# Performance work log

Hardware: AMD Instinct MI355X
Metric: run time of the kernel (lower is better)

Reference implementation:

```python
import jax, jax.numpy as jnp
import numpy as np

B = 1 << 20          # batch of independent integrator states
NC = 64              # RBF centers
DT = jnp.float32(0.005)
M_ = jnp.float32(1.0 / 95.45)
OFFST = jnp.float32(-3.2902)
F_V = jnp.float32(214.9261)
F_C = jnp.float32(19.3607)
A_COEF = (0.0, 0.5, 0.5, 1.0)  # RK stage offsets (module applies all to yddoti)


def setup_inputs() -> dict:
    key = jax.random.key(0)
    k1, k2, k3, k4, k5 = jax.random.split(key, 5)
    return {
        "inputs": jax.random.normal(k1, (B,), dtype=jnp.float32),     # control u per state
        "states": jax.random.normal(k2, (2, B), dtype=jnp.float32),   # ydot = states.view(2,-1)
        "centers": jax.random.normal(k3, (NC,), dtype=jnp.float32),
        "gammas": jax.random.uniform(k4, (NC,), dtype=jnp.float32),   # positive widths
        "weights": jax.random.normal(k5, (NC,), dtype=jnp.float32),
    }


def _rbf(x, centers, gammas, weights):
    # x: [B] -> Gaussian RBF features [B, NC] -> scalar output [B]
    d = x[:, None] - centers[None, :]
    phi = jnp.exp(-gammas[None, :] * d * d)
    return phi @ weights


def _fun(u, ydot, centers, gammas, weights):
    # (u_*u - F_v_@ydot - F_f_@ydot - C_*(offst + rbf(ydot[1]))) * M
    # row 0: -ydot[1];  row 1: u - F_v*ydot[1] - F_c*ydot[1] - (offst + rbf(ydot[1]))
    y1 = ydot[1]
    r = _rbf(y1, centers, gammas, weights)
    f0 = -y1
    f1 = u - F_V * y1 - F_C * y1 - (OFFST + r)
    return jnp.stack([f0, f1], axis=0) * M_


def reference(inputs, states, centers, gammas, weights):
    ydot = states.reshape(2, -1)  # [2, B]
    yddoti = _fun(inputs, ydot, centers, gammas, weights)
    # NOTE: faithful to source — every stage offsets from yddoti, not k_i
    ydoti = ydot + A_COEF[0] * yddoti * DT
    k1 = _fun(inputs, ydoti, centers, gammas, weights)
    ydot2 = ydot + A_COEF[1] * yddoti * DT
    k2 = _fun(inputs, ydot2, centers, gammas, weights)
    ydot3 = ydot + A_COEF[2] * yddoti * DT
    k3 = _fun(inputs, ydot3, centers, gammas, weights)
    ydot4 = ydot + A_COEF[3] * yddoti * DT
    k4 = _fun(inputs, ydot4, centers, gammas, weights)
    st_n = DT / 6.0 * (k1 + 2.0 * k2 + 2.0 * k3 + k4)
    return st_n  # [2, B]
```

## Files before the change

kernel.cpp:

```cpp
#include <hip/hip_runtime.h>


#define NTAB   256
#define XMIN   (-8.0f)
#define HSTEP  0.0625f
#define INVH   16.0f
#define TOFF   128.0f
#define SMAX   254.999f

__device__ __constant__ const float kM     = (float)(1.0 / 95.45);
__device__ __constant__ const float kOFFST = -3.2902f;
__device__ __constant__ const float kKK    = 214.9261f + 19.3607f;
__device__ __constant__ const float kC1    = (0.005f / 6.0f) * (float)(1.0 / 95.45);

__device__ __forceinline__ void rk_core(const float2* __restrict__ ltab,
                                        float u, float y1,
                                        float& o0, float& o1) {
    float s  = fmaf(y1, INVH, TOFF);
    s = fminf(fmaxf(s, 0.0f), SMAX);
    float fl = floorf(s);
    float fr = s - fl;
    float2 p = ltab[(int)fl];
    float r0 = fmaf(fr, p.y, p.x);
    float d1 = (fmaf(-kKK, y1, u) - (kOFFST + r0)) * kM;
    float t3 = (3.0f * 0.005f) * d1;
    float lin = fmaf(6.0f, y1, t3);
    o0 = -kC1 * lin;
    float rsum = fmaf(p.y * INVH, t3, 6.0f * r0);
    float acc  = fmaf(-kKK, lin, fmaf(6.0f, u, -6.0f * kOFFST)) - rsum;
    o1 = kC1 * acc;
}

template <int NC>
__global__ __launch_bounds__(256)
void rk_fused_kernel(const float* __restrict__ u_in,
                     const float* __restrict__ y1_in,
                     const float* __restrict__ centers,
                     const float* __restrict__ gammas,
                     const float* __restrict__ weights,
                     float* __restrict__ out, int B, int nc) {
    __shared__ float  vraw[NTAB];
    __shared__ float2 ltab[NTAB];
    const int tid = threadIdx.x;
    const long base = ((long)blockIdx.x * blockDim.x + tid) * 8;
    const bool full = (base + 8 <= (long)B);

    float4 ua, ub, ya, yb;
    if (full) {
        ua = *(const float4*)(u_in  + base);
        ub = *(const float4*)(u_in  + base + 4);
        ya = *(const float4*)(y1_in + base);
        yb = *(const float4*)(y1_in + base + 4);
    }

    {
        float x = XMIN + (float)tid * HSTEP;
        float v = 0.0f;
        if (NC > 0) {
            #pragma unroll
            for (int j = 0; j < NC; ++j) {
                float d = x - centers[j];
                v = fmaf(weights[j], __expf(-gammas[j] * d * d), v);
            }
        } else {
            for (int j = 0; j < nc; ++j) {
                float d = x - centers[j];
                v = fmaf(weights[j], __expf(-gammas[j] * d * d), v);
            }
        }
        vraw[tid] = v;
    }
    __syncthreads();
    {
        float v0 = vraw[tid];
        float sl = (tid < NTAB - 1) ? (vraw[tid + 1] - v0) : 0.0f;
        ltab[tid] = make_float2(v0, sl);
    }
    __syncthreads();

    if (full) {
        float uu[8] = {ua.x, ua.y, ua.z, ua.w, ub.x, ub.y, ub.z, ub.w};
        float yy[8] = {ya.x, ya.y, ya.z, ya.w, yb.x, yb.y, yb.z, yb.w};
        float o0[8], o1[8];
        #pragma unroll
        for (int e = 0; e < 8; ++e) rk_core(ltab, uu[e], yy[e], o0[e], o1[e]);
        *(float4*)(out + base)         = make_float4(o0[0], o0[1], o0[2], o0[3]);
        *(float4*)(out + base + 4)     = make_float4(o0[4], o0[5], o0[6], o0[7]);
        *(float4*)(out + B + base)     = make_float4(o1[0], o1[1], o1[2], o1[3]);
        *(float4*)(out + B + base + 4) = make_float4(o1[4], o1[5], o1[6], o1[7]);
    } else {
        for (long e = base; e < (long)B && e < base + 8; ++e) {
            float o0, o1;
            rk_core(ltab, u_in[e], y1_in[e], o0, o1);
            out[e] = o0;
            out[B + e] = o1;
        }
    }
}

extern "C" void kernel_launch(void* const* d_in, const int* in_sizes, int n_in,
                              void* d_out, int out_size, void* d_ws, size_t ws_size,
                              hipStream_t stream) {
    const float* u       = (const float*)d_in[0];
    const float* states  = (const float*)d_in[1];
    const float* centers = (const float*)d_in[2];
    const float* gammas  = (const float*)d_in[3];
    const float* weights = (const float*)d_in[4];
    int B  = in_sizes[0];
    int nc = in_sizes[2];
    const float* y1 = states + B;
    float* out = (float*)d_out;

    int nthreads = (B + 7) / 8;
    int nblocks  = (nthreads + 255) / 256;
    if (nc == 64) {
        rk_fused_kernel<64><<<nblocks, 256, 0, stream>>>(u, y1, centers, gammas,
                                                         weights, out, B, nc);
    } else {
        rk_fused_kernel<0><<<nblocks, 256, 0, stream>>>(u, y1, centers, gammas,
                                                        weights, out, B, nc);
    }
}
```

Before: 10.25 us.

## Double elements per thread and split LUT into separate value/slope arrays

Each thread now handles 16 elements instead of 8, halving the block count, so the per-block 256-entry RBF table build (64 exps per thread) is amortized over twice as much data. The interleaved float2 table is replaced by two separate float arrays, which removes the scratch copy but turns one 8-byte LDS gather into two 4-byte gathers. The risk is fewer blocks (256 for 1M elements on a 256-CU part), so each CU gets roughly one block, with more register pressure and less latency hiding.

```diff
diff --git a/kernel.cpp b/kernel.cpp
--- a/kernel.cpp
+++ b/kernel.cpp
@@ -1,5 +1,7 @@
 #include <hip/hip_runtime.h>
 
+
+typedef float v4f __attribute__((ext_vector_type(4)));
 
 #define NTAB   256
 #define XMIN   (-8.0f)
@@ -7,26 +9,30 @@
 #define INVH   16.0f
 #define TOFF   128.0f
 #define SMAX   254.999f
+#define EPT    16
 
 __device__ __constant__ const float kM     = (float)(1.0 / 95.45);
 __device__ __constant__ const float kOFFST = -3.2902f;
 __device__ __constant__ const float kKK    = 214.9261f + 19.3607f;
 __device__ __constant__ const float kC1    = (0.005f / 6.0f) * (float)(1.0 / 95.45);
 
-__device__ __forceinline__ void rk_core(const float2* __restrict__ ltab,
+__device__ __forceinline__ void rk_core(const float* __restrict__ lval,
+                                        const float* __restrict__ lslope,
                                         float u, float y1,
                                         float& o0, float& o1) {
     float s  = fmaf(y1, INVH, TOFF);
     s = fminf(fmaxf(s, 0.0f), SMAX);
     float fl = floorf(s);
     float fr = s - fl;
-    float2 p = ltab[(int)fl];
-    float r0 = fmaf(fr, p.y, p.x);
+    int   i  = (int)fl;
+    float pv = lval[i];
+    float ps = lslope[i];
+    float r0 = fmaf(fr, ps, pv);
     float d1 = (fmaf(-kKK, y1, u) - (kOFFST + r0)) * kM;
     float t3 = (3.0f * 0.005f) * d1;
     float lin = fmaf(6.0f, y1, t3);
     o0 = -kC1 * lin;
-    float rsum = fmaf(p.y * INVH, t3, 6.0f * r0);
+    float rsum = fmaf(ps * INVH, t3, 6.0f * r0);
     float acc  = fmaf(-kKK, lin, fmaf(6.0f, u, -6.0f * kOFFST)) - rsum;
     o1 = kC1 * acc;
 }
@@ -39,18 +45,19 @@
                      const float* __restrict__ gammas,
                      const float* __restrict__ weights,
                      float* __restrict__ out, int B, int nc) {
-    __shared__ float  vraw[NTAB];
-    __shared__ float2 ltab[NTAB];
+    __shared__ float lval[NTAB];
+    __shared__ float lslope[NTAB];
     const int tid = threadIdx.x;
-    const long base = ((long)blockIdx.x * blockDim.x + tid) * 8;
-    const bool full = (base + 8 <= (long)B);
+    const long base = ((long)blockIdx.x * blockDim.x + tid) * EPT;
+    const bool full = (base + EPT <= (long)B);
 
-    float4 ua, ub, ya, yb;
+    v4f uv[EPT / 4], yv[EPT / 4];
     if (full) {
-        ua = *(const float4*)(u_in  + base);
-        ub = *(const float4*)(u_in  + base + 4);
-        ya = *(const float4*)(y1_in + base);
-        yb = *(const float4*)(y1_in + base + 4);
+        #pragma unroll
+        for (int q = 0; q < EPT / 4; ++q) {
+            uv[q] = *(const v4f*)(u_in  + base + 4 * q);
+            yv[q] = *(const v4f*)(y1_in + base + 4 * q);
+        }
     }
 
     {
@@ -68,30 +75,34 @@
                 v = fmaf(weights[j], __expf(-gammas[j] * d * d), v);
             }
         }
-        vraw[tid] = v;
+        lval[tid] = v;
     }
     __syncthreads();
     {
-        float v0 = vraw[tid];
-        float sl = (tid < NTAB - 1) ? (vraw[tid + 1] - v0) : 0.0f;
-        ltab[tid] = make_float2(v0, sl);
+        float v0 = lval[tid];
+        float sl = (tid < NTAB - 1) ? (lval[tid + 1] - v0) : 0.0f;
+        lslope[tid] = sl;
     }
     __syncthreads();
 
     if (full) {
-        float uu[8] = {ua.x, ua.y, ua.z, ua.w, ub.x, ub.y, ub.z, ub.w};
-        float yy[8] = {ya.x, ya.y, ya.z, ya.w, yb.x, yb.y, yb.z, yb.w};
-        float o0[8], o1[8];
         #pragma unroll
-        for (int e = 0; e < 8; ++e) rk_core(ltab, uu[e], yy[e], o0[e], o1[e]);
-        *(float4*)(out + base)         = make_float4(o0[0], o0[1], o0[2], o0[3]);
-        *(float4*)(out + base + 4)     = make_float4(o0[4], o0[5], o0[6], o0[7]);
-        *(float4*)(out + B + base)     = make_float4(o1[0], o1[1], o1[2], o1[3]);
-        *(float4*)(out + B + base + 4) = make_float4(o1[4], o1[5], o1[6], o1[7]);
+        for (int q = 0; q < EPT / 4; ++q) {
+            float uu[4] = {uv[q].x, uv[q].y, uv[q].z, uv[q].w};
+            float yy[4] = {yv[q].x, yv[q].y, yv[q].z, yv[q].w};
+            float o0[4], o1[4];
+            #pragma unroll
+            for (int e = 0; e < 4; ++e)
+                rk_core(lval, lslope, uu[e], yy[e], o0[e], o1[e]);
+            v4f w0 = {o0[0], o0[1], o0[2], o0[3]};
+            v4f w1 = {o1[0], o1[1], o1[2], o1[3]};
+            *(v4f*)(out + base + 4 * q)     = w0;
+            *(v4f*)(out + B + base + 4 * q) = w1;
+        }
     } else {
-        for (long e = base; e < (long)B && e < base + 8; ++e) {
+        for (long e = base; e < (long)B && e < base + EPT; ++e) {
             float o0, o1;
-            rk_core(ltab, u_in[e], y1_in[e], o0, o1);
+            rk_core(lval, lslope, u_in[e], y1_in[e], o0, o1);
             out[e] = o0;
             out[B + e] = o1;
         }
@@ -111,7 +122,7 @@
     const float* y1 = states + B;
     float* out = (float*)d_out;
 
-    int nthreads = (B + 7) / 8;
+    int nthreads = (B + EPT - 1) / EPT;
     int nblocks  = (nthreads + 255) / 256;
     if (nc == 64) {
         rk_fused_kernel<64><<<nblocks, 256, 0, stream>>>(u, y1, centers, gammas,
```

New measurement: 13.88 us. 1.35x slower.
